# Performance work log

Measured on AMD Instinct MI355X. Metric: run time of the kernel, lower is better.

## Reference

```python
import jax, jax.numpy as jnp
import numpy as np

C = 768
R = 16
H = C // R  # 48


def setup_inputs() -> dict:
    key = jax.random.key(0)
    ks = jax.random.split(key, 5)
    x = jax.random.normal(ks[0], (32, 64, 64, C), dtype=jnp.float32)
    # Xavier-uniform linear weights (stored as [in, out] for jnp.dot)
    lim1 = float(np.sqrt(6.0 / (C + H)))
    W1 = jax.random.uniform(ks[1], (C, H), dtype=jnp.float32, minval=-lim1, maxval=lim1)
    b1 = jax.random.normal(ks[2], (H,), dtype=jnp.float32) * 1e-6
    lim2 = float(np.sqrt(6.0 / (H + C)))
    W2 = jax.random.uniform(ks[3], (H, C), dtype=jnp.float32, minval=-lim2, maxval=lim2)
    b2 = jax.random.normal(ks[4], (C,), dtype=jnp.float32) * 1e-6
    gamma = jnp.ones((C,), dtype=jnp.float32)
    beta = jnp.zeros((C,), dtype=jnp.float32)
    return {"x": x, "W1": W1, "b1": b1, "W2": W2, "b2": b2, "gamma": gamma, "beta": beta}


def _layernorm(x, gamma, beta, eps=1e-5):
    mu = jnp.mean(x, axis=-1, keepdims=True)
    var = jnp.mean(jnp.square(x - mu), axis=-1, keepdims=True)
    return (x - mu) * jax.lax.rsqrt(var + eps) * gamma + beta


def reference(x, W1, b1, W2, b2, gamma, beta):
    # x: [b, h, w, c]; LayerNorm over c, bottleneck MLP, residual add.
    out1 = _layernorm(x, gamma, beta)
    hid = out1 @ W1 + b1                       # [b,h,w,H]
    hid = hid * jax.nn.sigmoid(1.702 * hid)    # QuickGELU
    out = hid @ W2 + b2                        # [b,h,w,c]
    return x + out
```

## Files before the change

kernel.cpp:

```cpp
#include <hip/hip_runtime.h>
#include <hip/hip_bf16.h>
#include <stdint.h>

#define CDIM 768
#define HDIM 48

typedef float  f32x4  __attribute__((ext_vector_type(4)));
typedef short  bf16x8 __attribute__((ext_vector_type(8)));
typedef unsigned short u16x4 __attribute__((ext_vector_type(4)));

__device__ __forceinline__ unsigned short f2bf(float x) {
    __hip_bfloat16 h = __float2bfloat16(x);
    return *reinterpret_cast<unsigned short*>(&h);
}
#define SB0() __builtin_amdgcn_sched_barrier(0)

__device__ __forceinline__ void gload_lds16(const void* g, void* l) {
    __builtin_amdgcn_global_load_lds(
        (const __attribute__((address_space(1))) unsigned int*)g,
        (__attribute__((address_space(3))) unsigned int*)l, 16, 0, 0);
}

__global__ __launch_bounds__(256) void prep_kernel(
    const float* __restrict__ W1, const float* __restrict__ b1,
    const float* __restrict__ W2,
    const float* __restrict__ gamma, const float* __restrict__ beta,
    unsigned short* __restrict__ w1p, unsigned short* __restrict__ w2p,
    float* __restrict__ b1p, float* __restrict__ cs1)
{
    const int blk = blockIdx.x, tid = threadIdx.x;
    const int l = tid & 63;
    if (blk < 18) {
        const int fid = blk * 4 + (tid >> 6);
        const int kt = fid / 3, nt = fid % 3;
        const int k0 = kt * 32 + 8 * (l >> 4);
        const int n  = nt * 16 + (l & 15);
        bf16x8 v;
        #pragma unroll
        for (int b = 0; b < 8; ++b) {
            const int k = k0 + b;
            v[b] = (short)f2bf(gamma[k] * W1[k * HDIM + n]);
        }
        *reinterpret_cast<bf16x8*>(w1p + (size_t)(fid * 64 + l) * 8) = v;
    } else if (blk < 42) {
        const int fid = (blk - 18) * 4 + (tid >> 6);
        const int kt = fid / 48, nt = fid % 48;
        const int k0 = kt * 32 + 8 * (l >> 4);
        const int n  = nt * 16 + (l & 15);
        bf16x8 v;
        #pragma unroll
        for (int b = 0; b < 8; ++b) {
            const int k = k0 + b;
            const float w = (k < HDIM) ? W2[k * CDIM + n] : 0.0f;
            v[b] = (short)f2bf(w);
        }
        *reinterpret_cast<bf16x8*>(w2p + (size_t)(fid * 64 + l) * 8) = v;
    } else {
        const int j = tid >> 2, p = tid & 3;
        float sb = 0.f, sg = 0.f;
        if (j < HDIM) {
            for (int c = p * 192; c < (p + 1) * 192; ++c) {
                const float w = W1[c * HDIM + j];
                sb += beta[c]  * w;
                sg += gamma[c] * w;
            }
        }
        sb += __shfl_xor(sb, 1); sb += __shfl_xor(sb, 2);
        sg += __shfl_xor(sg, 1); sg += __shfl_xor(sg, 2);
        if (p == 0 && j < HDIM) { b1p[j] = b1[j] + sb; cs1[j] = sg; }
    }
}

__global__ __launch_bounds__(256, 2) void mlp_kernel(
    const float* __restrict__ x,
    const float* __restrict__ b2g,
    const unsigned short* __restrict__ w1p,
    const unsigned short* __restrict__ w2p,
    const float* __restrict__ b1p,
    const float* __restrict__ cs1,
    float* __restrict__ out)
{
    __shared__ __align__(16) float lds_x[4][4096];
    __shared__ __align__(16) float lds_b2[CDIM];
    __shared__ __align__(16) float lds_b1[HDIM];
    __shared__ __align__(16) float lds_cs[HDIM];

    const int tid  = threadIdx.x;
    const int w    = tid >> 6;
    const int l    = tid & 63;
    const int lrow = l & 15;
    const int lg   = l >> 4;

    if (tid < 192)       reinterpret_cast<f32x4*>(lds_b2)[tid]       = reinterpret_cast<const f32x4*>(b2g)[tid];
    else if (tid < 204)  reinterpret_cast<f32x4*>(lds_b1)[tid - 192] = reinterpret_cast<const f32x4*>(b1p)[tid - 192];
    else if (tid < 216)  reinterpret_cast<f32x4*>(lds_cs)[tid - 204] = reinterpret_cast<const f32x4*>(cs1)[tid - 204];
    __syncthreads();

    const bf16x8* __restrict__ w1f = reinterpret_cast<const bf16x8*>(w1p);
    const bf16x8* __restrict__ w2f = reinterpret_cast<const bf16x8*>(w2p);

    const int    tile = blockIdx.x * 4 + w;
    const size_t m0   = (size_t)tile * 16;

    char* const wavebuf = (char*)&lds_x[w][0];
    const char* const xg = (const char*)x + m0 * 3072;

    int srcoff[8];
    #pragma unroll
    for (int j = 0; j < 8; ++j) {
        const int r = 2 * j + (l >> 5);
        srcoff[j] = r * 3072 + ((((l & 31) ^ (r & 7))) << 4);
    }

    bf16x8 wq[2][12];
    #pragma unroll
    for (int i = 0; i < 2; ++i) {
        #pragma unroll
        for (int q = 0; q < 12; ++q) wq[i][q] = w1f[(i * 12 + q) * 64 + l];
        #pragma unroll
        for (int j = 0; j < 8; ++j)
            gload_lds16(xg + i * 512 + srcoff[j], wavebuf + i * 8192 + j * 1024);
    }
    SB0();

    const int rowb = lrow * 512;
    const int rx   = (lrow & 7) << 4;

    f32x4 acc1[3];
    #pragma unroll
    for (int nt = 0; nt < 3; ++nt) { acc1[nt][0]=0.f; acc1[nt][1]=0.f; acc1[nt][2]=0.f; acc1[nt][3]=0.f; }
    float rsum = 0.f, rsq = 0.f;

    #pragma unroll
    for (int cc = 0; cc < 6; ++cc) {
        if (cc < 5) asm volatile("s_waitcnt vmcnt(20)" ::: "memory");
        else        asm volatile("s_waitcnt vmcnt(0)" ::: "memory");
        bf16x8 wv[12];
        #pragma unroll
        for (int q = 0; q < 12; ++q) wv[q] = wq[cc & 1][q];
        const char* bb = wavebuf + (cc & 1) * 8192 + rowb;
        f32x4 xr[8];
        #pragma unroll
        for (int ktl = 0; ktl < 4; ++ktl) {
            xr[2*ktl+0] = *reinterpret_cast<const f32x4*>(bb + ((ktl * 128 + lg * 32     ) ^ rx));
            xr[2*ktl+1] = *reinterpret_cast<const f32x4*>(bb + ((ktl * 128 + lg * 32 + 16) ^ rx));
        }
        asm volatile("s_waitcnt lgkmcnt(0)" ::: "memory");
        SB0();
        if (cc + 2 < 6) {
            #pragma unroll
            for (int q = 0; q < 12; ++q)
                wq[cc & 1][q] = w1f[((cc + 2) * 12 + q) * 64 + l];
            #pragma unroll
            for (int j = 0; j < 8; ++j)
                gload_lds16(xg + (cc + 2) * 512 + srcoff[j], wavebuf + (cc & 1) * 8192 + j * 1024);
        }
        SB0();
        #pragma unroll
        for (int ktl = 0; ktl < 4; ++ktl) {
            const f32x4 xa = xr[2*ktl+0];
            const f32x4 xb = xr[2*ktl+1];
            bf16x8 bf;
            #pragma unroll
            for (int b = 0; b < 4; ++b) {
                rsum += xa[b]; rsq += xa[b] * xa[b];
                rsum += xb[b]; rsq += xb[b] * xb[b];
                bf[b]     = (short)f2bf(xa[b]);
                bf[b + 4] = (short)f2bf(xb[b]);
            }
            acc1[0] = __builtin_amdgcn_mfma_f32_16x16x32_bf16(wv[ktl*3+0], bf, acc1[0], 0, 0, 0);
            acc1[1] = __builtin_amdgcn_mfma_f32_16x16x32_bf16(wv[ktl*3+1], bf, acc1[1], 0, 0, 0);
            acc1[2] = __builtin_amdgcn_mfma_f32_16x16x32_bf16(wv[ktl*3+2], bf, acc1[2], 0, 0, 0);
        }
    }

    rsum += __shfl_xor(rsum, 16); rsum += __shfl_xor(rsum, 32);
    rsq  += __shfl_xor(rsq , 16); rsq  += __shfl_xor(rsq , 32);
    const float mu   = rsum * (1.f / 768.f);
    const float var  = rsq * (1.f / 768.f) - mu * mu;
    const float rstd = rsqrtf(var + 1e-5f);

    unsigned short* const hid = (unsigned short*)wavebuf;
    *reinterpret_cast<unsigned long long*>(hid + (l >> 2) * 72 + 48 + (l & 3) * 4) = 0ull;
    #pragma unroll
    for (int nt = 0; nt < 3; ++nt) {
        const int c4 = nt * 16 + 4 * lg;
        const f32x4 bb = *reinterpret_cast<const f32x4*>(&lds_b1[c4]);
        const f32x4 cs = *reinterpret_cast<const f32x4*>(&lds_cs[c4]);
        u16x4 pk;
        #pragma unroll
        for (int r = 0; r < 4; ++r) {
            const float h = rstd * (acc1[nt][r] - mu * cs[r]) + bb[r];
            const float g = h / (1.f + __expf(-1.702f * h));
            pk[r] = f2bf(g);
        }
        *reinterpret_cast<u16x4*>(hid + lrow * 72 + c4) = pk;
    }
    const bf16x8 a2_0 = *reinterpret_cast<const bf16x8*>(hid + lrow * 72 + 8 * lg);
    const bf16x8 a2_1 = *reinterpret_cast<const bf16x8*>(hid + lrow * 72 + 8 * lg + 32);

    const float* __restrict__ xres = x   + (m0 + lrow) * CDIM;
    float* __restrict__       ores = out + (m0 + lrow) * CDIM;

    #pragma unroll 1
    for (int ch = 0; ch < 6; ++ch) {
        f32x4 res[8];
        #pragma unroll
        for (int n8 = 0; n8 < 8; ++n8)
            res[n8] = *reinterpret_cast<const f32x4*>(xres + (ch * 8 + n8) * 16 + 4 * lg);
        f32x4 acc2[8];
        #pragma unroll
        for (int n8 = 0; n8 < 8; ++n8) { acc2[n8][0]=0.f; acc2[n8][1]=0.f; acc2[n8][2]=0.f; acc2[n8][3]=0.f; }
        #pragma unroll
        for (int n8 = 0; n8 < 8; ++n8) {
            const int ct = ch * 8 + n8;
            acc2[n8] = __builtin_amdgcn_mfma_f32_16x16x32_bf16(w2f[ct * 64 + l],        a2_0, acc2[n8], 0, 0, 0);
            acc2[n8] = __builtin_amdgcn_mfma_f32_16x16x32_bf16(w2f[(48 + ct) * 64 + l], a2_1, acc2[n8], 0, 0, 0);
        }
        #pragma unroll
        for (int n8 = 0; n8 < 8; ++n8) {
            const int c4 = (ch * 8 + n8) * 16 + 4 * lg;
            const f32x4 bb = *reinterpret_cast<const f32x4*>(&lds_b2[c4]);
            f32x4 o;
            #pragma unroll
            for (int r = 0; r < 4; ++r) o[r] = acc2[n8][r] + bb[r] + res[n8][r];
            *reinterpret_cast<f32x4*>(ores + c4) = o;
        }
    }
}

extern "C" void kernel_launch(void* const* d_in, const int* in_sizes, int n_in,
                              void* d_out, int out_size, void* d_ws, size_t ws_size,
                              hipStream_t stream)
{
    const float* x     = (const float*)d_in[0];
    const float* W1    = (const float*)d_in[1];
    const float* b1    = (const float*)d_in[2];
    const float* W2    = (const float*)d_in[3];
    const float* b2    = (const float*)d_in[4];
    const float* gamma = (const float*)d_in[5];
    const float* beta  = (const float*)d_in[6];
    float* out = (float*)d_out;

    unsigned short* w1p = (unsigned short*)d_ws;
    unsigned short* w2p = w1p + 24 * 3 * 64 * 8;
    float* b1p = (float*)(w2p + 2 * 48 * 64 * 8);
    float* cs1 = b1p + 64;

    const int M = in_sizes[0] / CDIM;
    const int blocks = M / 64;

    prep_kernel<<<dim3(43), dim3(256), 0, stream>>>(W1, b1, W2, gamma, beta, w1p, w2p, b1p, cs1);
    mlp_kernel<<<dim3(blocks), dim3(256), 0, stream>>>(x, b2, w1p, w2p, b1p, cs1, out);
}
```

Measured before the change: 275.0 us.

## Split fused MLP into separate GEMM1 and GEMM2 kernels via workspace hidden buffer

Splits the fused LayerNorm+MLP kernel into two kernels: one computes the normalized first GEMM plus QuickGELU and writes a bf16 hidden tensor to workspace, the second does the second GEMM, bias and residual. Each kernel gets lower register/LDS pressure and gemm2 can run at higher occupancy. It adds a global round-trip for the hidden tensor and a second full read of x in a separate launch, and falls back to the fused kernel if workspace is too small.

```diff
diff --git a/kernel.cpp b/kernel.cpp
--- a/kernel.cpp
+++ b/kernel.cpp
@@ -71,7 +71,184 @@
     }
 }
 
-__global__ __launch_bounds__(256, 2) void mlp_kernel(
+__global__ __launch_bounds__(256, 2) void gemm1_kernel(
+    const float* __restrict__ x,
+    const unsigned short* __restrict__ w1p,
+    const float* __restrict__ b1p,
+    const float* __restrict__ cs1,
+    unsigned short* __restrict__ hidp)
+{
+    __shared__ __align__(16) float lds_x[4][4096];
+    __shared__ __align__(16) float lds_b1[HDIM];
+    __shared__ __align__(16) float lds_cs[HDIM];
+
+    const int tid  = threadIdx.x;
+    const int w    = tid >> 6;
+    const int l    = tid & 63;
+    const int lrow = l & 15;
+    const int lg   = l >> 4;
+
+    if (tid < 12)       reinterpret_cast<f32x4*>(lds_b1)[tid]      = reinterpret_cast<const f32x4*>(b1p)[tid];
+    else if (tid < 24)  reinterpret_cast<f32x4*>(lds_cs)[tid - 12] = reinterpret_cast<const f32x4*>(cs1)[tid - 12];
+    __syncthreads();
+
+    const bf16x8* __restrict__ w1f = reinterpret_cast<const bf16x8*>(w1p);
+    const int    tile = blockIdx.x * 4 + w;
+    const size_t m0   = (size_t)tile * 16;
+
+    char* const wavebuf = (char*)&lds_x[w][0];
+    const char* const xg = (const char*)x + m0 * 3072;
+
+    int srcoff[8];
+    #pragma unroll
+    for (int j = 0; j < 8; ++j) {
+        const int r = 2 * j + (l >> 5);
+        srcoff[j] = r * 3072 + ((((l & 31) ^ (r & 7))) << 4);
+    }
+
+    bf16x8 wq[2][12];
+    #pragma unroll
+    for (int i = 0; i < 2; ++i) {
+        #pragma unroll
+        for (int q = 0; q < 12; ++q) wq[i][q] = w1f[(i * 12 + q) * 64 + l];
+        #pragma unroll
+        for (int j = 0; j < 8; ++j)
+            gload_lds16(xg + i * 512 + srcoff[j], wavebuf + i * 8192 + j * 1024);
+    }
+    SB0();
+
+    const int rowb = lrow * 512;
+    const int rx   = (lrow & 7) << 4;
+
+    f32x4 acc1[3];
+    #pragma unroll
+    for (int nt = 0; nt < 3; ++nt) { acc1[nt][0]=0.f; acc1[nt][1]=0.f; acc1[nt][2]=0.f; acc1[nt][3]=0.f; }
+    float rsum = 0.f, rsq = 0.f;
+
+    #pragma unroll
+    for (int cc = 0; cc < 6; ++cc) {
+        if (cc < 5) asm volatile("s_waitcnt vmcnt(20)" ::: "memory");
+        else        asm volatile("s_waitcnt vmcnt(0)" ::: "memory");
+        bf16x8 wv[12];
+        #pragma unroll
+        for (int q = 0; q < 12; ++q) wv[q] = wq[cc & 1][q];
+        const char* bb = wavebuf + (cc & 1) * 8192 + rowb;
+        f32x4 xr[8];
+        #pragma unroll
+        for (int ktl = 0; ktl < 4; ++ktl) {
+            xr[2*ktl+0] = *reinterpret_cast<const f32x4*>(bb + ((ktl * 128 + lg * 32     ) ^ rx));
+            xr[2*ktl+1] = *reinterpret_cast<const f32x4*>(bb + ((ktl * 128 + lg * 32 + 16) ^ rx));
+        }
+        asm volatile("s_waitcnt lgkmcnt(0)" ::: "memory");
+        SB0();
+        if (cc + 2 < 6) {
+            #pragma unroll
+            for (int q = 0; q < 12; ++q)
+                wq[cc & 1][q] = w1f[((cc + 2) * 12 + q) * 64 + l];
+            #pragma unroll
+            for (int j = 0; j < 8; ++j)
+                gload_lds16(xg + (cc + 2) * 512 + srcoff[j], wavebuf + (cc & 1) * 8192 + j * 1024);
+        }
+        SB0();
+        #pragma unroll
+        for (int ktl = 0; ktl < 4; ++ktl) {
+            const f32x4 xa = xr[2*ktl+0];
+            const f32x4 xb = xr[2*ktl+1];
+            bf16x8 bf;
+            #pragma unroll
+            for (int b = 0; b < 4; ++b) {
+                rsum += xa[b]; rsq += xa[b] * xa[b];
+                rsum += xb[b]; rsq += xb[b] * xb[b];
+                bf[b]     = (short)f2bf(xa[b]);
+                bf[b + 4] = (short)f2bf(xb[b]);
+            }
+            acc1[0] = __builtin_amdgcn_mfma_f32_16x16x32_bf16(wv[ktl*3+0], bf, acc1[0], 0, 0, 0);
+            acc1[1] = __builtin_amdgcn_mfma_f32_16x16x32_bf16(wv[ktl*3+1], bf, acc1[1], 0, 0, 0);
+            acc1[2] = __builtin_amdgcn_mfma_f32_16x16x32_bf16(wv[ktl*3+2], bf, acc1[2], 0, 0, 0);
+        }
+    }
+
+    rsum += __shfl_xor(rsum, 16); rsum += __shfl_xor(rsum, 32);
+    rsq  += __shfl_xor(rsq , 16); rsq  += __shfl_xor(rsq , 32);
+    const float mu   = rsum * (1.f / 768.f);
+    const float var  = rsq * (1.f / 768.f) - mu * mu;
+    const float rstd = rsqrtf(var + 1e-5f);
+
+    unsigned short* const hrow = hidp + (m0 + lrow) * 64;
+    #pragma unroll
+    for (int nt = 0; nt < 3; ++nt) {
+        const int c4 = nt * 16 + 4 * lg;
+        const f32x4 bb = *reinterpret_cast<const f32x4*>(&lds_b1[c4]);
+        const f32x4 cs = *reinterpret_cast<const f32x4*>(&lds_cs[c4]);
+        u16x4 pk;
+        #pragma unroll
+        for (int r = 0; r < 4; ++r) {
+            const float h = rstd * (acc1[nt][r] - mu * cs[r]) + bb[r];
+            const float g = h / (1.f + __expf(-1.702f * h));
+            pk[r] = f2bf(g);
+        }
+        *reinterpret_cast<u16x4*>(hrow + c4) = pk;
+    }
+    u16x4 z; z[0]=0; z[1]=0; z[2]=0; z[3]=0;
+    *reinterpret_cast<u16x4*>(hrow + 48 + 4 * lg) = z;
+}
+
+__global__ __launch_bounds__(256, 4) void gemm2_kernel(
+    const float* __restrict__ x,
+    const unsigned short* __restrict__ hidp,
+    const float* __restrict__ b2g,
+    const unsigned short* __restrict__ w2p,
+    float* __restrict__ out)
+{
+    __shared__ __align__(16) float lds_b2[CDIM];
+    const int tid  = threadIdx.x;
+    const int w    = tid >> 6;
+    const int l    = tid & 63;
+    const int lrow = l & 15;
+    const int lg   = l >> 4;
+
+    if (tid < 192) reinterpret_cast<f32x4*>(lds_b2)[tid] = reinterpret_cast<const f32x4*>(b2g)[tid];
+    __syncthreads();
+
+    const bf16x8* __restrict__ w2f = reinterpret_cast<const bf16x8*>(w2p);
+    const int    tile = blockIdx.x * 4 + w;
+    const size_t m0   = (size_t)tile * 16;
+
+    const unsigned short* const hrow = hidp + (m0 + lrow) * 64;
+    const bf16x8 a2_0 = *reinterpret_cast<const bf16x8*>(hrow + 8 * lg);
+    const bf16x8 a2_1 = *reinterpret_cast<const bf16x8*>(hrow + 32 + 8 * lg);
+
+    const float* __restrict__ xres = x   + (m0 + lrow) * CDIM;
+    float* __restrict__       ores = out + (m0 + lrow) * CDIM;
+
+    #pragma unroll 1
+    for (int ch = 0; ch < 6; ++ch) {
+        f32x4 res[8];
+        #pragma unroll
+        for (int n8 = 0; n8 < 8; ++n8)
+            res[n8] = *reinterpret_cast<const f32x4*>(xres + (ch * 8 + n8) * 16 + 4 * lg);
+        f32x4 acc2[8];
+        #pragma unroll
+        for (int n8 = 0; n8 < 8; ++n8) { acc2[n8][0]=0.f; acc2[n8][1]=0.f; acc2[n8][2]=0.f; acc2[n8][3]=0.f; }
+        #pragma unroll
+        for (int n8 = 0; n8 < 8; ++n8) {
+            const int ct = ch * 8 + n8;
+            acc2[n8] = __builtin_amdgcn_mfma_f32_16x16x32_bf16(w2f[ct * 64 + l],        a2_0, acc2[n8], 0, 0, 0);
+            acc2[n8] = __builtin_amdgcn_mfma_f32_16x16x32_bf16(w2f[(48 + ct) * 64 + l], a2_1, acc2[n8], 0, 0, 0);
+        }
+        #pragma unroll
+        for (int n8 = 0; n8 < 8; ++n8) {
+            const int c4 = (ch * 8 + n8) * 16 + 4 * lg;
+            const f32x4 bb = *reinterpret_cast<const f32x4*>(&lds_b2[c4]);
+            f32x4 o;
+            #pragma unroll
+            for (int r = 0; r < 4; ++r) o[r] = acc2[n8][r] + bb[r] + res[n8][r];
+            *reinterpret_cast<f32x4*>(ores + c4) = o;
+        }
+    }
+}
+
+__global__ __launch_bounds__(256, 2) void mlp_fused_kernel(
     const float* __restrict__ x,
     const float* __restrict__ b2g,
     const unsigned short* __restrict__ w1p,
@@ -98,20 +275,17 @@
 
     const bf16x8* __restrict__ w1f = reinterpret_cast<const bf16x8*>(w1p);
     const bf16x8* __restrict__ w2f = reinterpret_cast<const bf16x8*>(w2p);
-
     const int    tile = blockIdx.x * 4 + w;
     const size_t m0   = (size_t)tile * 16;
 
     char* const wavebuf = (char*)&lds_x[w][0];
     const char* const xg = (const char*)x + m0 * 3072;
-
     int srcoff[8];
     #pragma unroll
     for (int j = 0; j < 8; ++j) {
         const int r = 2 * j + (l >> 5);
         srcoff[j] = r * 3072 + ((((l & 31) ^ (r & 7))) << 4);
     }
-
     bf16x8 wq[2][12];
     #pragma unroll
     for (int i = 0; i < 2; ++i) {
@@ -122,15 +296,12 @@
             gload_lds16(xg + i * 512 + srcoff[j], wavebuf + i * 8192 + j * 1024);
     }
     SB0();
-
     const int rowb = lrow * 512;
     const int rx   = (lrow & 7) << 4;
-
     f32x4 acc1[3];
     #pragma unroll
     for (int nt = 0; nt < 3; ++nt) { acc1[nt][0]=0.f; acc1[nt][1]=0.f; acc1[nt][2]=0.f; acc1[nt][3]=0.f; }
     float rsum = 0.f, rsq = 0.f;
-
     #pragma unroll
     for (int cc = 0; cc < 6; ++cc) {
         if (cc < 5) asm volatile("s_waitcnt vmcnt(20)" ::: "memory");
@@ -173,13 +344,11 @@
             acc1[2] = __builtin_amdgcn_mfma_f32_16x16x32_bf16(wv[ktl*3+2], bf, acc1[2], 0, 0, 0);
         }
     }
-
     rsum += __shfl_xor(rsum, 16); rsum += __shfl_xor(rsum, 32);
     rsq  += __shfl_xor(rsq , 16); rsq  += __shfl_xor(rsq , 32);
     const float mu   = rsum * (1.f / 768.f);
     const float var  = rsq * (1.f / 768.f) - mu * mu;
     const float rstd = rsqrtf(var + 1e-5f);
-
     unsigned short* const hid = (unsigned short*)wavebuf;
     *reinterpret_cast<unsigned long long*>(hid + (l >> 2) * 72 + 48 + (l & 3) * 4) = 0ull;
     #pragma unroll
@@ -198,10 +367,8 @@
     }
     const bf16x8 a2_0 = *reinterpret_cast<const bf16x8*>(hid + lrow * 72 + 8 * lg);
     const bf16x8 a2_1 = *reinterpret_cast<const bf16x8*>(hid + lrow * 72 + 8 * lg + 32);
-
     const float* __restrict__ xres = x   + (m0 + lrow) * CDIM;
     float* __restrict__       ores = out + (m0 + lrow) * CDIM;
-
     #pragma unroll 1
     for (int ch = 0; ch < 6; ++ch) {
         f32x4 res[8];
@@ -251,5 +418,14 @@
     const int blocks = M / 64;
 
     prep_kernel<<<dim3(43), dim3(256), 0, stream>>>(W1, b1, W2, gamma, beta, w1p, w2p, b1p, cs1);
-    mlp_kernel<<<dim3(blocks), dim3(256), 0, stream>>>(x, b2, w1p, w2p, b1p, cs1, out);
-}
+
+    const size_t hid_off  = 262144;
+    const size_t hid_need = hid_off + (size_t)M * 64 * 2;
+    if (ws_size >= hid_need) {
+        unsigned short* hidp = (unsigned short*)((char*)d_ws + hid_off);
+        gemm1_kernel<<<dim3(blocks), dim3(256), 0, stream>>>(x, w1p, b1p, cs1, hidp);
+        gemm2_kernel<<<dim3(blocks), dim3(256), 0, stream>>>(x, hidp, b2, w2p, out);
+    } else {
+        mlp_fused_kernel<<<dim3(blocks), dim3(256), 0, stream>>>(x, b2, w1p, w2p, b1p, cs1, out);
+    }
+}
```

Result: slower. 437.9 us (+59.2%).
